# Kernel tuning notes

Measured on AMD Instinct MI355X. Metric: run time of the kernel, lower is better.

Reference implementation:

```python
import jax, jax.numpy as jnp
import numpy as np
import math

D_MODEL = 512; NHEAD = 8; D_HEAD = 64; C_OUT = 64
SEQ_LEN = 1024; PRED_LEN = 256; K = 8; DIM_FF = 2048
LOW_FREQ = 1; EPS = 1e-5
BATCH = 8


def _next_fast_len(n):
    # smallest 5-smooth integer >= n (matches scipy.fftpack.next_fast_len)
    while True:
        m = n
        for p in (2, 3, 5):
            while m % p == 0:
                m //= p
        if m == 1:
            return n
        n += 1


def _conv1d_fft(f, g, n):
    # matches torch conv1d_fft with N == M == n along axis 1 (cross-correlation via conj)
    fast_len = _next_fast_len(2 * n - 1)
    Ff = jnp.fft.rfft(f, n=fast_len, axis=1)
    Fg = jnp.fft.rfft(g, n=fast_len, axis=1)
    out = jnp.fft.irfft(Ff * jnp.conj(Fg), n=fast_len, axis=1)
    out = jnp.roll(out, -1, axis=1)
    return out[:, fast_len - n:fast_len]


def _exp_smooth(values, sw, v0, aux_values=None):
    # values: (b,t,h,d); sw: (h,1); v0: (1,1,h,d or 1)
    b, t, h, d = values.shape
    alpha = jax.nn.sigmoid(sw)                        # (h,1)
    powers = jnp.arange(t, dtype=values.dtype)
    weight = (1.0 - alpha) * alpha ** powers[::-1]    # (h,t)
    init_w = alpha ** (powers + 1.0)                  # (h,t)
    weight = weight.T[None, :, :, None]               # (1,t,h,1)
    init_w = init_w.T[None, :, :, None]
    out = init_w * v0 + _conv1d_fft(values, weight, t)
    if aux_values is not None:
        aux_w = weight * (alpha / (1.0 - alpha))[None, None, :, :]
        out = out + _conv1d_fft(aux_values, aux_w, t)
    return out


def _layer_norm(x, g, b):
    mu = x.mean(-1, keepdims=True)
    var = ((x - mu) ** 2).mean(-1, keepdims=True)
    return (x - mu) * jax.lax.rsqrt(var + EPS) * g + b


def _fourier_season(x):
    b, t, d = x.shape
    xf = jnp.fft.rfft(x, axis=1)                      # (b, t//2+1, d) complex
    hi = xf.shape[1] - 1 if t % 2 == 0 else xf.shape[1]
    xf = xf[:, LOW_FREQ:hi]                           # (b, F, d)
    freqs = (jnp.arange(t // 2 + 1, dtype=x.dtype) / t)[LOW_FREQ:hi]
    # top-K frequencies per (batch, feature) by amplitude
    _, idx = jax.lax.top_k(jnp.abs(jnp.moveaxis(xf, 1, 2)), K)   # (b,d,K)
    idx = jnp.moveaxis(idx, 2, 1)                     # (b,K,d)
    x_sel = jnp.take_along_axis(xf, idx, axis=1)      # (b,K,d) complex
    f_sel = freqs[idx]                                # (b,K,d)
    # trig re-synthesis / extrapolation over t + PRED_LEN steps
    x_all = jnp.concatenate([x_sel, jnp.conj(x_sel)], axis=1)    # (b,2K,d)
    f_all = jnp.concatenate([f_sel, -f_sel], axis=1)[:, :, None, :]  # (b,2K,1,d)
    t_val = jnp.arange(t + PRED_LEN, dtype=x.dtype).reshape(1, 1, -1, 1)
    amp = (jnp.abs(x_all) / t)[:, :, None, :]
    phase = jnp.angle(x_all)[:, :, None, :]
    x_time = amp * jnp.cos(2.0 * math.pi * f_all * t_val + phase)  # (b,2K,T,d)
    return x_time.sum(axis=1)                         # (b, t+PRED_LEN, d)


def _growth_layer(x, z0, in_w, in_b, sw, v0, out_w, out_b):
    b, t, _ = x.shape
    v = (x @ in_w.T + in_b).reshape(b, t, NHEAD, D_HEAD)
    v = jnp.concatenate([jnp.broadcast_to(z0[None, None], (b, 1, NHEAD, D_HEAD)), v], axis=1)
    v = v[:, 1:] - v[:, :-1]                          # first differences, (b,t,h,dh)
    s = _exp_smooth(v, sw, v0)
    s = jnp.concatenate([jnp.broadcast_to(v0, (b, 1, NHEAD, D_HEAD)), s], axis=1)  # (b,t+1,h,dh)
    return s.reshape(b, t + 1, NHEAD * D_HEAD) @ out_w.T + out_b


def _level_layer(level, growth, season, sw, v0, gw, gb, spw, spb):
    b, t, _ = level.shape
    g = (growth @ gw.T + gb)[..., None]               # (b,t,c,1)
    s = (season @ spw.T + spb)[..., None]             # (b,t,c,1)
    l = level[..., None] - s
    out = _exp_smooth(l, sw, v0, aux_values=g)        # (b,t,c,1)
    return out[..., 0]


def _forward(res, level, gl_z0, gl_in_w, gl_in_b, gl_sw, gl_v0, gl_out_w, gl_out_b,
             ll_sw, ll_v0, ll_gw, ll_gb, ll_sw2, ll_sb, ff_w1, ff_w2,
             n1_g, n1_b, n2_g, n2_b):
    season = _fourier_season(res)                     # (b, t+P, d)
    res = res - season[:, :-PRED_LEN]
    growth = _growth_layer(res, gl_z0, gl_in_w, gl_in_b, gl_sw, gl_v0, gl_out_w, gl_out_b)  # (b,t+1,d)
    res = _layer_norm(res - growth[:, 1:], n1_g, n1_b)
    ff = jax.nn.sigmoid(res @ ff_w1.T) @ ff_w2.T      # Feedforward, activation='sigmoid', no bias
    res = _layer_norm(res + ff, n2_g, n2_b)
    level = _level_layer(level, growth[:, :-1], season[:, :-PRED_LEN],
                         ll_sw, ll_v0, ll_gw, ll_gb, ll_sw2, ll_sb)
    return res, level, growth, season


def setup_inputs() -> dict:
    key = jax.random.key(0)
    ks = jax.random.split(key, 16)
    f32 = jnp.float32
    rn = lambda k, shape, s=1.0: jax.random.normal(k, shape, dtype=f32) * s
    return {
        "res": rn(ks[0], (BATCH, SEQ_LEN, D_MODEL)),
        "level": rn(ks[1], (BATCH, SEQ_LEN, C_OUT)),
        "gl_z0": rn(ks[2], (NHEAD, D_HEAD)),
        "gl_in_w": rn(ks[3], (NHEAD * D_HEAD, D_MODEL), 0.02),
        "gl_in_b": jnp.zeros((NHEAD * D_HEAD,), f32),
        "gl_sw": rn(ks[4], (NHEAD, 1)),
        "gl_v0": rn(ks[5], (1, 1, NHEAD, D_HEAD)),
        "gl_out_w": rn(ks[6], (D_MODEL, NHEAD * D_HEAD), 0.02),
        "gl_out_b": jnp.zeros((D_MODEL,), f32),
        "ll_sw": rn(ks[7], (C_OUT, 1)),
        "ll_v0": rn(ks[8], (1, 1, C_OUT, 1)),
        "ll_gw": rn(ks[9], (C_OUT, D_MODEL), 0.02),
        "ll_gb": jnp.zeros((C_OUT,), f32),
        "ll_sw2": rn(ks[10], (C_OUT, D_MODEL), 0.02),
        "ll_sb": jnp.zeros((C_OUT,), f32),
        "ff_w1": rn(ks[11], (DIM_FF, D_MODEL), 0.02),
        "ff_w2": rn(ks[12], (D_MODEL, DIM_FF), 0.02),
        "n1_g": jnp.ones((D_MODEL,), f32),
        "n1_b": jnp.zeros((D_MODEL,), f32),
        "n2_g": jnp.ones((D_MODEL,), f32),
        "n2_b": jnp.zeros((D_MODEL,), f32),
    }


def reference(res, level, gl_z0, gl_in_w, gl_in_b, gl_sw, gl_v0, gl_out_w, gl_out_b,
              ll_sw, ll_v0, ll_gw, ll_gb, ll_sw2, ll_sb, ff_w1, ff_w2,
              n1_g, n1_b, n2_g, n2_b):
    return _forward(res, level, gl_z0, gl_in_w, gl_in_b, gl_sw, gl_v0, gl_out_w, gl_out_b,
                    ll_sw, ll_v0, ll_gw, ll_gb, ll_sw2, ll_sb, ff_w1, ff_w2,
                    n1_g, n1_b, n2_g, n2_b)
```

## Files before the change

### kernel.cpp

```cpp
#include <hip/hip_runtime.h>
#include <hip/hip_bf16.h>
#include <math.h>

#define B_ 8
#define T_ 1024
#define D_ 512
#define PRED 256
#define TP (T_ + PRED)
#define NH 8
#define DH 64
#define DFF 2048
#define CO 64
#define KSEL 8

typedef __hip_bfloat16 bf16;
using bf16x8 = __attribute__((ext_vector_type(8))) short;
using f32x4  = __attribute__((ext_vector_type(4))) float;

__device__ __forceinline__ void gload_lds16(const void* gp, void* lp) {
  __builtin_amdgcn_global_load_lds(
      (const __attribute__((address_space(1))) void*)gp,
      (__attribute__((address_space(3))) void*)lp, 16, 0, 0);
}

template <int N>
__device__ __forceinline__ void vm_wait() {
  if constexpr (N == 0)      asm volatile("s_waitcnt vmcnt(0)" ::: "memory");
  else if constexpr (N == 2) asm volatile("s_waitcnt vmcnt(2)" ::: "memory");
  else if constexpr (N == 4) asm volatile("s_waitcnt vmcnt(4)" ::: "memory");
  else if constexpr (N == 6) asm volatile("s_waitcnt vmcnt(6)" ::: "memory");
  else if constexpr (N == 8) asm volatile("s_waitcnt vmcnt(8)" ::: "memory");
  else static_assert(N == 0, "unsupported vmcnt literal");
}

__global__ __launch_bounds__(256) void k_transpose(const float* __restrict__ in, float* __restrict__ out) {
  __shared__ float tile[32][33];
  const int b = blockIdx.z;
  const int d0 = blockIdx.x * 32, t0 = blockIdx.y * 32;
  const int tx = threadIdx.x, ty = threadIdx.y;
  const float* src = in + ((size_t)b * T_ + t0) * D_ + d0;
#pragma unroll
  for (int i = 0; i < 32; i += 8) tile[ty + i][tx] = src[(size_t)(ty + i) * D_ + tx];
  __syncthreads();
  float* dst = out + ((size_t)b * D_ + d0) * T_ + t0;
#pragma unroll
  for (int i = 0; i < 32; i += 8) dst[(size_t)(ty + i) * T_ + tx] = tile[tx][ty + i];
}

__global__ __launch_bounds__(256) void k_fft_topk(const float* __restrict__ xt, float* __restrict__ comp) {
  __shared__ float2 bufA[2][512], bufB[2][512];
  __shared__ float2 tw[384];
  __shared__ float wvv[2][2][4];
  __shared__ int wkk[2][2][4];
  __shared__ int selk[2][KSEL];
  float* const mg0 = (float*)&bufA[0][0];
  float* const mg1 = (float*)&bufA[1][0];
  const int j = threadIdx.x;
  const size_t bd0 = (size_t)blockIdx.x * 2;
  {
    const float c = -6.283185307179586f / 512.0f;
    tw[j] = make_float2(__cosf(c * (float)j), __sinf(c * (float)j));
    if (j < 128) tw[256 + j] = make_float2(__cosf(c * (float)(256 + j)), __sinf(c * (float)(256 + j)));
  }
  const float4 u0 = ((const float4*)(xt + bd0 * 1024))[j];
  const float4 u1 = ((const float4*)(xt + (bd0 + 1) * 1024))[j];
  bufA[0][2 * j] = make_float2(u0.x, u0.y); bufA[0][2 * j + 1] = make_float2(u0.z, u0.w);
  bufA[1][2 * j] = make_float2(u1.x, u1.y); bufA[1][2 * j + 1] = make_float2(u1.z, u1.w);
  __syncthreads();
  {
    const float2 w = tw[j];
#pragma unroll
    for (int sx2 = 0; sx2 < 2; ++sx2) {
      const float2 a = bufA[sx2][j], b = bufA[sx2][j + 256];
      bufB[sx2][2 * j] = make_float2(a.x + b.x, a.y + b.y);
      const float ex = a.x - b.x, ey = a.y - b.y;
      bufB[sx2][2 * j + 1] = make_float2(ex * w.x - ey * w.y, ex * w.y + ey * w.x);
    }
  }
  __syncthreads();
  const int sx = j >> 7, idx = j & 127;
#pragma unroll
  for (int st = 0; st < 4; ++st) {
    const int lg = 1 + 2 * st;
    const int s = 1 << lg;
    const int p = idx >> lg;
    const int q = idx & (s - 1);
    const float2* src = (st & 1) ? (const float2*)bufA[sx] : (const float2*)bufB[sx];
    float2* dst = (st & 1) ? (float2*)bufB[sx] : (float2*)bufA[sx];
    const float2 x0 = src[idx];
    const float2 x1 = src[idx + 128];
    const float2 x2 = src[idx + 256];
    const float2 x3 = src[idx + 384];
    const float2 e0 = make_float2(x0.x + x2.x, x0.y + x2.y);
    const float2 e1 = make_float2(x0.x - x2.x, x0.y - x2.y);
    const float2 e2 = make_float2(x1.x + x3.x, x1.y + x3.y);
    const float2 e3 = make_float2(x1.x - x3.x, x1.y - x3.y);
    const float2 y0 = make_float2(e0.x + e2.x, e0.y + e2.y);
    const float2 y2 = make_float2(e0.x - e2.x, e0.y - e2.y);
    const float2 y1 = make_float2(e1.x + e3.y, e1.y - e3.x);
    const float2 y3 = make_float2(e1.x - e3.y, e1.y + e3.x);
    const int spi = p << lg;
    const float2 w1 = tw[spi], w2 = tw[2 * spi], w3 = tw[3 * spi];
    const int ob = q + (p << (lg + 2));
    dst[ob] = y0;
    dst[ob + s] = make_float2(y1.x * w1.x - y1.y * w1.y, y1.x * w1.y + y1.y * w1.x);
    dst[ob + 2 * s] = make_float2(y2.x * w2.x - y2.y * w2.y, y2.x * w2.y + y2.y * w2.x);
    dst[ob + 3 * s] = make_float2(y3.x * w3.x - y3.y * w3.y, y3.x * w3.y + y3.y * w3.x);
    __syncthreads();
  }
#pragma unroll
  for (int u = 0; u < 2; ++u) {
    const int k = (u == 0) ? (j + 1) : (j + 257);
    if (k <= 511) {
#pragma unroll
      for (int s2 = 0; s2 < 2; ++s2) {
        const float2 zk = bufB[s2][k & 511];
        const float2 zm = bufB[s2][(512 - k) & 511];
        const float Ex = 0.5f * (zk.x + zm.x), Ey = 0.5f * (zk.y - zm.y);
        const float Ox = 0.5f * (zk.y + zm.y), Oy = 0.5f * (zm.x - zk.x);
        const float ang = -(6.283185307179586f / 1024.0f) * (float)k;
        const float cs = __cosf(ang), sn = __sinf(ang);
        const float Xr = Ex + cs * Ox - sn * Oy;
        const float Xi = Ey + cs * Oy + sn * Ox;
        ((s2 == 0) ? mg0 : mg1)[k] = Xr * Xr + Xi * Xi;
      }
    }
  }
  __syncthreads();
  float a0 = mg0[j], b0v = mg0[j + 256];
  float a1 = mg1[j], b1v = mg1[j + 256];
  if (j == 0) { a0 = -1.0f; a1 = -1.0f; }
  const int lane = j & 63, wvi = j >> 6;
  for (int r = 0; r < KSEL; ++r) {
    const int par = r & 1;
    float bv0 = a0; int bk0 = j;
    if (b0v > bv0) { bv0 = b0v; bk0 = j + 256; }
    float bv1 = a1; int bk1 = j;
    if (b1v > bv1) { bv1 = b1v; bk1 = j + 256; }
#pragma unroll
    for (int off = 32; off; off >>= 1) {
      const float ov0 = __shfl_down(bv0, off); const int ok0 = __shfl_down(bk0, off);
      if (ov0 > bv0 || (ov0 == bv0 && ok0 < bk0)) { bv0 = ov0; bk0 = ok0; }
      const float ov1 = __shfl_down(bv1, off); const int ok1 = __shfl_down(bk1, off);
      if (ov1 > bv1 || (ov1 == bv1 && ok1 < bk1)) { bv1 = ov1; bk1 = ok1; }
    }
    if (lane == 0) {
      wvv[0][par][wvi] = bv0; wkk[0][par][wvi] = bk0;
      wvv[1][par][wvi] = bv1; wkk[1][par][wvi] = bk1;
    }
    __syncthreads();
    float fv0 = wvv[0][par][0]; int fk0 = wkk[0][par][0];
    float fv1 = wvv[1][par][0]; int fk1 = wkk[1][par][0];
#pragma unroll
    for (int i = 1; i < 4; i++) {
      if (wvv[0][par][i] > fv0 || (wvv[0][par][i] == fv0 && wkk[0][par][i] < fk0)) { fv0 = wvv[0][par][i]; fk0 = wkk[0][par][i]; }
      if (wvv[1][par][i] > fv1 || (wvv[1][par][i] == fv1 && wkk[1][par][i] < fk1)) { fv1 = wvv[1][par][i]; fk1 = wkk[1][par][i]; }
    }
    if (j == 0) { selk[0][r] = fk0; selk[1][r] = fk1; }
    if (fk0 == j) a0 = -2.0f;
    if (fk0 == j + 256) b0v = -2.0f;
    if (fk1 == j) a1 = -2.0f;
    if (fk1 == j + 256) b1v = -2.0f;
  }
  __syncthreads();
  if (j < 2 * KSEL) {
    const int s2 = j >> 3, r = j & 7;
    const int k = selk[s2][r];
    const float2 zk = bufB[s2][k & 511];
    const float2 zm = bufB[s2][(512 - k) & 511];
    const float Ex = 0.5f * (zk.x + zm.x), Ey = 0.5f * (zk.y - zm.y);
    const float Ox = 0.5f * (zk.y + zm.y), Oy = 0.5f * (zm.x - zk.x);
    const float ang = -(6.283185307179586f / 1024.0f) * (float)k;
    const float cs = __cosf(ang), sn = __sinf(ang);
    const float Xr = Ex + cs * Ox - sn * Oy;
    const float Xi = Ey + cs * Oy + sn * Ox;
    float* o = comp + (bd0 + s2) * 24 + r * 3;
    o[0] = 2.0f * sqrtf(Xr * Xr + Xi * Xi) * (1.0f / 1024.0f);
    o[1] = (float)k;
    o[2] = atan2f(Xi, Xr);
  }
}

__global__ __launch_bounds__(512) void k_season(const float* __restrict__ comp, const float* __restrict__ res,
                                                float* __restrict__ season, bf16* __restrict__ res1b,
                                                bf16* __restrict__ seasb) {
  const int d = threadIdx.x;
  const int b = blockIdx.y;
  const int t0 = blockIdx.x * 5;
  float a_[8], kf_[8], ph_[8];
  const float* c = comp + ((size_t)b * 512 + d) * 24;
#pragma unroll
  for (int i = 0; i < 8; i++) { a_[i] = c[3 * i]; kf_[i] = c[3 * i + 1]; ph_[i] = c[3 * i + 2]; }
#pragma unroll
  for (int tt = 0; tt < 5; ++tt) {
    const int t = t0 + tt;
    float acc = 0.0f;
#pragma unroll
    for (int i = 0; i < 8; i++) {
      float fr = kf_[i] * (float)t * (1.0f / 1024.0f);
      fr -= floorf(fr);
      acc += a_[i] * __cosf(fmaf(6.283185307179586f, fr, ph_[i]));
    }
    season[((size_t)b * TP + t) * D_ + d] = acc;
    if (t < T_) {
      const float rr = res[((size_t)b * T_ + t) * D_ + d] - acc;
      res1b[((size_t)b * T_ + t) * D_ + d] = __float2bfloat16(rr);
      seasb[((size_t)b * T_ + t) * D_ + d] = __float2bfloat16(acc);
    }
  }
}

#define CVT_TOTAL 2686976
__global__ __launch_bounds__(256) void k_cvt_all(const float* __restrict__ s0, const float* __restrict__ s1,
                                                 const float* __restrict__ s2_, const float* __restrict__ s3,
                                                 const float* __restrict__ s4, const float* __restrict__ s5,
                                                 bf16* __restrict__ dst) {
  const int i = (blockIdx.x * 256 + threadIdx.x) * 4;
  if (i >= CVT_TOTAL) return;
  const float* src;
  int off;
  if (i < 262144)       { src = s0;  off = i; }
  else if (i < 524288)  { src = s1;  off = i - 262144; }
  else if (i < 1572864) { src = s2_; off = i - 524288; }
  else if (i < 2621440) { src = s3;  off = i - 1572864; }
  else if (i < 2654208) { src = s4;  off = i - 2621440; }
  else                  { src = s5;  off = i - 2654208; }
  const float4 v = *(const float4*)(src + off);
  bf16* o = dst + i;
  o[0] = __float2bfloat16(v.x); o[1] = __float2bfloat16(v.y);
  o[2] = __float2bfloat16(v.z); o[3] = __float2bfloat16(v.w);
}

__global__ __launch_bounds__(1024) void k_growth_scan2(const float* __restrict__ v, const float* __restrict__ z0,
                                                       const float* __restrict__ sw, const float* __restrict__ v0,
                                                       bf16* __restrict__ s2) {
  const int b = blockIdx.x >> 3;
  const int col = (blockIdx.x & 7) * 64 + (threadIdx.x & 63);
  const int w = threadIdx.x >> 6;
  const float alpha = 1.0f / (1.0f + expf(-sw[col >> 6]));
  const float om = 1.0f - alpha;
  float a64 = alpha;
#pragma unroll
  for (int i = 0; i < 6; i++) a64 *= a64;
  const float* vp = v + (size_t)b * T_ * D_ + col;
  float vprev = (w == 0) ? z0[col] : vp[(size_t)(64 * w - 1) * D_];
  float sloc = 0.0f;
#pragma unroll 8
  for (int j = 0; j < 64; j++) {
    const float nv = vp[(size_t)(64 * w + j) * D_];
    sloc = alpha * sloc + om * (nv - vprev);
    vprev = nv;
  }
  __shared__ float lb[16][64], lc[16][64];
  lb[w][threadIdx.x & 63] = sloc;
  __syncthreads();
  if (w == 0) {
    float s = v0[col];
#pragma unroll
    for (int k = 0; k < 16; k++) { lc[k][threadIdx.x & 63] = s; s = a64 * s + lb[k][threadIdx.x & 63]; }
  }
  __syncthreads();
  float s = lc[w][threadIdx.x & 63];
  vprev = (w == 0) ? z0[col] : vp[(size_t)(64 * w - 1) * D_];
  bf16* op = s2 + (size_t)b * (T_ + 1) * D_ + col;
  if (w == 0) op[0] = __float2bfloat16(v0[col]);
#pragma unroll 8
  for (int j = 0; j < 64; j++) {
    const float nv = vp[(size_t)(64 * w + j) * D_];
    s = alpha * s + om * (nv - vprev);
    vprev = nv;
    op[(size_t)(64 * w + j + 1) * D_] = __float2bfloat16(s);
  }
}

__global__ __launch_bounds__(1024) void k_level_scan2(const float* __restrict__ level, const float* __restrict__ gp,
                                                      const float* __restrict__ sp, const float* __restrict__ sw,
                                                      const float* __restrict__ v0, float* __restrict__ out) {
  const int b = blockIdx.x;
  const int w = threadIdx.x >> 6;
  const int c = threadIdx.x & 63;
  const float alpha = 1.0f / (1.0f + expf(-sw[c]));
  const float om = 1.0f - alpha;
  float a64 = alpha;
#pragma unroll
  for (int i = 0; i < 6; i++) a64 *= a64;
  const size_t base = ((size_t)b * T_ + 64 * w) * CO + c;
  float sloc = 0.0f;
#pragma unroll 8
  for (int j = 0; j < 64; j++) {
    const size_t idx = base + (size_t)j * CO;
    const float u = om * (level[idx] - sp[idx]) + alpha * gp[idx];
    out[idx] = u;
    sloc = alpha * sloc + u;
  }
  __shared__ float lb[16][64], lc[16][64];
  lb[w][c] = sloc;
  __syncthreads();
  if (w == 0) {
    float s = v0[c];
#pragma unroll
    for (int k = 0; k < 16; k++) { lc[k][c] = s; s = a64 * s + lb[k][c]; }
  }
  __syncthreads();
  float s = lc[w][c];
#pragma unroll 8
  for (int j = 0; j < 64; j++) {
    const size_t idx = base + (size_t)j * CO;
    s = alpha * s + out[idx];
    out[idx] = s;
  }
}

template <int MODE>
__global__ __launch_bounds__(128) void k_ln(const float* __restrict__ x1, const bf16* __restrict__ xb,
                                            const float* __restrict__ x3, const float* __restrict__ g,
                                            const float* __restrict__ be, float* __restrict__ outF,
                                            bf16* __restrict__ outB) {
  const int m = blockIdx.x, tid = threadIdx.x;
  const int b = m >> 10;
  float4 v;
  if (MODE == 0) {
    const ushort4 rb = ((const ushort4*)(xb + (size_t)m * D_))[tid];
    const float4 gr = ((const float4*)(x3 + ((size_t)(m + b + 1)) * D_))[tid];
    v.x = __uint_as_float((unsigned)rb.x << 16) - gr.x;
    v.y = __uint_as_float((unsigned)rb.y << 16) - gr.y;
    v.z = __uint_as_float((unsigned)rb.z << 16) - gr.z;
    v.w = __uint_as_float((unsigned)rb.w << 16) - gr.w;
  } else {
    v = ((const float4*)(x1 + (size_t)m * D_))[tid];
  }
  float s = v.x + v.y + v.z + v.w;
  float s2 = v.x * v.x + v.y * v.y + v.z * v.z + v.w * v.w;
#pragma unroll
  for (int off = 32; off; off >>= 1) { s += __shfl_down(s, off); s2 += __shfl_down(s2, off); }
  __shared__ float p1[2], p2[2];
  if ((tid & 63) == 0) { p1[tid >> 6] = s; p2[tid >> 6] = s2; }
  __syncthreads();
  const float S = p1[0] + p1[1], S2 = p2[0] + p2[1];
  const float mu = S * (1.0f / 512.0f);
  const float rs = rsqrtf(fmaxf(S2 * (1.0f / 512.0f) - mu * mu, 0.0f) + 1e-5f);
  const float4 gg = ((const float4*)g)[tid], bb = ((const float4*)be)[tid];
  float4 o;
  o.x = (v.x - mu) * rs * gg.x + bb.x;
  o.y = (v.y - mu) * rs * gg.y + bb.y;
  o.z = (v.z - mu) * rs * gg.z + bb.z;
  o.w = (v.w - mu) * rs * gg.w + bb.w;
  ((float4*)(outF + (size_t)m * D_))[tid] = o;
  if (MODE == 0) {
    bf16* ob = outB + (size_t)m * D_ + tid * 4;
    ob[0] = __float2bfloat16(o.x); ob[1] = __float2bfloat16(o.y);
    ob[2] = __float2bfloat16(o.z); ob[3] = __float2bfloat16(o.w);
  }
}

template <int BM, int BN, int BK, int WM, int WN, int EPI, bool DUAL = false>
__global__ __launch_bounds__(WM * WN * 64, 2) void k_gemm(
    const bf16* __restrict__ A, const bf16* __restrict__ Bw,
    const float* __restrict__ bias, float* outF, bf16* __restrict__ outB,
    const float* resid, const int M, const int N, const int K, int extra,
    const bf16* __restrict__ A2, const bf16* __restrict__ Bw2,
    const float* __restrict__ bias2, float* outF2, int extra2) {
  constexpr int NW = WM * WN;
  constexpr int FM = BM / (WM * 16);
  constexpr int FN = BN / (WN * 16);
  constexpr int RPC = 512 / BK;
  constexpr int LA = (BM / RPC) / NW, LB = (BN / RPC) / NW;
  constexpr int KK = BK / 32;
  constexpr int TLOADS = LA + LB;
  static_assert(LA >= 1 && LB >= 1, "tile too small for staging split");
  static_assert((BM / RPC) % NW == 0 && (BN / RPC) % NW == 0, "staging split");
  if constexpr (DUAL) {
    if (blockIdx.z == 1) { A = A2; Bw = Bw2; bias = bias2; outF = outF2; extra = extra2; }
  }
  __shared__ bf16 lsA[2][BM * BK];
  __shared__ bf16 lsB[2][BN * BK];
  const int tid = threadIdx.x;
  const int w = tid >> 6, lane = tid & 63;
  const int tm = blockIdx.x, tn = blockIdx.y;
  const int wr = w / WN, wc = w % WN;
  const int r16 = lane & 15, hi = lane >> 4;

  int srowoff, scoloff;
  if constexpr (BK == 64) {
    const int rr = lane >> 3, cs = lane & 7;
    srowoff = rr;
    scoloff = (cs ^ rr) * 8;
  } else {
    const int sr = lane >> 3, cs = lane & 7;
    const int idx = cs ^ (sr & 7);
    srowoff = sr * 2 + (idx >> 2);
    scoloff = (idx & 3) * 8;
  }

  const f32x4 fzero = {0.f, 0.f, 0.f, 0.f};
  f32x4 acc[FM][FN];
#pragma unroll
  for (int i = 0; i < FM; i++)
#pragma unroll
    for (int jj = 0; jj < FN; jj++) acc[i][jj] = fzero;

  const int NT = K / BK;

  auto stage = [&](int kt, int sel) {
#pragma unroll
    for (int q = 0; q < LA; q++) {
      const int g = w * LA + q;
      int m = tm * BM + g * RPC + srowoff;
      if (m > M - 1) m = M - 1;
      m += (m >> 10) * extra;
      gload_lds16(A + (size_t)m * K + (size_t)kt * BK + scoloff, &lsA[sel][g * 512]);
    }
#pragma unroll
    for (int q = 0; q < LB; q++) {
      const int g = w * LB + q;
      const int n = tn * BN + g * RPC + srowoff;
      gload_lds16(Bw + (size_t)n * K + (size_t)kt * BK + scoloff, &lsB[sel][g * 512]);
    }
  };

  auto frag = [&](const bf16* ls, int row, int cc) -> bf16x8 {
    if constexpr (BK == 64) {
      const int g = row >> 3, rr = row & 7;
      return *(const bf16x8*)&ls[g * 512 + rr * 64 + ((cc ^ rr) << 3)];
    } else {
      const int g = row >> 4, rr = row & 15, sr = rr >> 1;
      const int idx = ((rr & 1) << 2) | cc;
      return *(const bf16x8*)&ls[g * 512 + sr * 64 + ((idx ^ (sr & 7)) << 3)];
    }
  };

  stage(0, 0);
  for (int kt = 0; kt < NT; ++kt) {
    const int sel = kt & 1;
    if (kt + 1 < NT) {
      stage(kt + 1, sel ^ 1);
      vm_wait<TLOADS>();
    } else {
      vm_wait<0>();
    }
    __builtin_amdgcn_sched_barrier(0);
    __builtin_amdgcn_s_barrier();
    __builtin_amdgcn_sched_barrier(0);
#pragma unroll
    for (int kk = 0; kk < KK; ++kk) {
      bf16x8 af[FM], bfv[FN];
#pragma unroll
      for (int i = 0; i < FM; i++)
        af[i] = frag(lsA[sel], wr * (FM * 16) + i * 16 + r16, kk * 4 + hi);
#pragma unroll
      for (int jj = 0; jj < FN; jj++)
        bfv[jj] = frag(lsB[sel], wc * (FN * 16) + jj * 16 + r16, kk * 4 + hi);
#pragma unroll
      for (int i = 0; i < FM; i++)
#pragma unroll
        for (int jj = 0; jj < FN; jj++)
          acc[i][jj] = __builtin_amdgcn_mfma_f32_16x16x32_bf16(af[i], bfv[jj], acc[i][jj], 0, 0, 0);
    }
    if (kt + 1 < NT) {
      __builtin_amdgcn_sched_barrier(0);
      __builtin_amdgcn_s_barrier();
      __builtin_amdgcn_sched_barrier(0);
    }
  }

#pragma unroll
  for (int i = 0; i < FM; i++) {
#pragma unroll
    for (int r = 0; r < 4; r++) {
      const int m = tm * BM + wr * (FM * 16) + i * 16 + hi * 4 + r;
      if (m < M) {
#pragma unroll
        for (int jj = 0; jj < FN; jj++) {
          const int n = tn * BN + wc * (FN * 16) + jj * 16 + r16;
          float x = acc[i][jj][r];
          if (bias) x += bias[n];
          const size_t idx = (size_t)m * N + n;
          if (EPI == 0) {
            outF[idx] = x;
          } else if (EPI == 1) {
            outF[idx] = x;
            outB[idx] = __float2bfloat16(x);
          } else if (EPI == 2) {
            outB[idx] = __float2bfloat16(1.0f / (1.0f + __expf(-x)));
          } else {
            outF[idx] = x + resid[idx];
          }
        }
      }
    }
  }
}

#define MB (size_t)(1u << 20)
static const size_t OFF_A = 0;
static const size_t OFF_C = 32 * MB;
static const size_t OFF_D = 40 * MB;
static const size_t OFF_E = 48 * MB;
static const size_t OFF_F = 54 * MB;
static const size_t OFF_G = 63 * MB;
static const size_t OFF_H = 72 * MB;
static const size_t OFF_J = 88 * MB;
static const size_t OFF_K = 89 * MB;
static const size_t OFF_K2 = 91 * MB;

#define W_IN 0
#define W_OUT 262144
#define W_FF1 524288
#define W_FF2 1572864
#define W_GW 2621440
#define W_SW2 2654208

extern "C" void kernel_launch(void* const* d_in, const int* in_sizes, int n_in, void* d_out, int out_size,
                              void* d_ws, size_t ws_size, hipStream_t stream) {
  (void)in_sizes; (void)n_in; (void)out_size; (void)ws_size;
  const float* res = (const float*)d_in[0];
  const float* level = (const float*)d_in[1];
  const float* gl_z0 = (const float*)d_in[2];
  const float* gl_in_w = (const float*)d_in[3];
  const float* gl_in_b = (const float*)d_in[4];
  const float* gl_sw = (const float*)d_in[5];
  const float* gl_v0 = (const float*)d_in[6];
  const float* gl_out_w = (const float*)d_in[7];
  const float* gl_out_b = (const float*)d_in[8];
  const float* ll_sw = (const float*)d_in[9];
  const float* ll_v0 = (const float*)d_in[10];
  const float* ll_gw = (const float*)d_in[11];
  const float* ll_gb = (const float*)d_in[12];
  const float* ll_sw2 = (const float*)d_in[13];
  const float* ll_sb = (const float*)d_in[14];
  const float* ff_w1 = (const float*)d_in[15];
  const float* ff_w2 = (const float*)d_in[16];
  const float* n1_g = (const float*)d_in[17];
  const float* n1_b = (const float*)d_in[18];
  const float* n2_g = (const float*)d_in[19];
  const float* n2_b = (const float*)d_in[20];

  char* ws = (char*)d_ws;
  float* resT = (float*)(ws + OFF_A);
  float* vbuf = (float*)(ws + OFF_A);
  bf16* hbuf = (bf16*)(ws + OFF_A);
  bf16* res1b = (bf16*)(ws + OFF_C);
  bf16* res2b = (bf16*)(ws + OFF_C);
  bf16* seasb = (bf16*)(ws + OFF_D);
  bf16* wE = (bf16*)(ws + OFF_E);
  bf16* s2b = (bf16*)(ws + OFF_F);
  bf16* grob = (bf16*)(ws + OFF_G);
  float* res2f = (float*)(ws + OFF_H);
  float* comp = (float*)(ws + OFF_J);
  float* gproj = (float*)(ws + OFF_K);
  float* sproj = (float*)(ws + OFF_K2);

  float* o_res = (float*)d_out;
  float* o_level = o_res + 4194304;
  float* o_growth = o_level + 524288;
  float* o_season = o_growth + 4198400;

  k_transpose<<<dim3(16, 32, 8), dim3(32, 8), 0, stream>>>(res, resT);
  k_fft_topk<<<2048, 256, 0, stream>>>(resT, comp);
  k_season<<<dim3(256, 8), 512, 0, stream>>>(comp, res, o_season, res1b, seasb);
  k_cvt_all<<<(CVT_TOTAL / 4 + 255) / 256, 256, 0, stream>>>(gl_in_w, gl_out_w, ff_w1, ff_w2, ll_gw, ll_sw2, wE);
  k_gemm<64, 128, 64, 2, 2, 0><<<dim3(128, 4), 256, 0, stream>>>(
      res1b, wE + W_IN, gl_in_b, vbuf, nullptr, nullptr, 8192, 512, 512, 0,
      nullptr, nullptr, nullptr, nullptr, 0);
  k_growth_scan2<<<64, 1024, 0, stream>>>(vbuf, gl_z0, gl_sw, gl_v0, s2b);
  k_gemm<64, 128, 64, 2, 2, 1><<<dim3(129, 4), 256, 0, stream>>>(
      s2b, wE + W_OUT, gl_out_b, o_growth, grob, nullptr, 8200, 512, 512, 0,
      nullptr, nullptr, nullptr, nullptr, 0);
  k_ln<0><<<8192, 128, 0, stream>>>(nullptr, res1b, o_growth, n1_g, n1_b, res2f, res2b);
  k_gemm<128, 128, 32, 2, 2, 2><<<dim3(64, 16), 256, 0, stream>>>(
      res2b, wE + W_FF1, nullptr, nullptr, hbuf, nullptr, 8192, 2048, 512, 0,
      nullptr, nullptr, nullptr, nullptr, 0);
  k_gemm<64, 128, 64, 2, 2, 3><<<dim3(128, 4), 256, 0, stream>>>(
      hbuf, wE + W_FF2, nullptr, res2f, nullptr, res2f, 8192, 512, 2048, 0,
      nullptr, nullptr, nullptr, nullptr, 0);
  k_ln<1><<<8192, 128, 0, stream>>>(res2f, nullptr, nullptr, n2_g, n2_b, o_res, nullptr);
  k_gemm<64, 64, 64, 4, 1, 0, true><<<dim3(128, 1, 2), 256, 0, stream>>>(
      grob, wE + W_GW, ll_gb, gproj, nullptr, nullptr, 8192, 64, 512, 1,
      seasb, wE + W_SW2, ll_sb, sproj, 0);
  k_level_scan2<<<8, 1024, 0, stream>>>(level, gproj, sproj, ll_sw, ll_v0, o_level);
}
```

Baseline: 216.4 us.

## Fuse level-layer dual projections into one concatenated-K GEMM with folded scaling

The growth and season bf16 activations are written interleaved into one buffer of row width 1024, and the two projection weights are concatenated along K, pre-scaled by alpha and -(1-alpha). A single K=1024 GEMM with a new epilogue then computes the level-smoothing input u directly. This removes the second GEMM half, the separate gproj/sproj buffers and the first-pass elementwise work in the level scan. LayerNorm 1 now reads the growth output as bf16 from the shared buffer rather than fp32, which cuts read traffic but adds rounding.

```diff
diff --git a/kernel.cpp b/kernel.cpp
--- a/kernel.cpp
+++ b/kernel.cpp
@@ -183,7 +183,7 @@
 
 __global__ __launch_bounds__(512) void k_season(const float* __restrict__ comp, const float* __restrict__ res,
                                                 float* __restrict__ season, bf16* __restrict__ res1b,
-                                                bf16* __restrict__ seasb) {
+                                                bf16* __restrict__ seasC) {
   const int d = threadIdx.x;
   const int b = blockIdx.y;
   const int t0 = blockIdx.x * 5;
@@ -205,7 +205,7 @@
     if (t < T_) {
       const float rr = res[((size_t)b * T_ + t) * D_ + d] - acc;
       res1b[((size_t)b * T_ + t) * D_ + d] = __float2bfloat16(rr);
-      seasb[((size_t)b * T_ + t) * D_ + d] = __float2bfloat16(acc);
+      seasC[((size_t)b * 1025 + t) * 1024 + 512 + d] = __float2bfloat16(acc);
     }
   }
 }
@@ -214,21 +214,33 @@
 __global__ __launch_bounds__(256) void k_cvt_all(const float* __restrict__ s0, const float* __restrict__ s1,
                                                  const float* __restrict__ s2_, const float* __restrict__ s3,
                                                  const float* __restrict__ s4, const float* __restrict__ s5,
-                                                 bf16* __restrict__ dst) {
+                                                 const float* __restrict__ llsw, bf16* __restrict__ dst) {
   const int i = (blockIdx.x * 256 + threadIdx.x) * 4;
   if (i >= CVT_TOTAL) return;
   const float* src;
   int off;
+  float scale = 1.0f;
+  int di = i;
   if (i < 262144)       { src = s0;  off = i; }
   else if (i < 524288)  { src = s1;  off = i - 262144; }
   else if (i < 1572864) { src = s2_; off = i - 524288; }
   else if (i < 2621440) { src = s3;  off = i - 1572864; }
-  else if (i < 2654208) { src = s4;  off = i - 2621440; }
-  else                  { src = s5;  off = i - 2654208; }
+  else if (i < 2654208) {
+    src = s4;  off = i - 2621440;
+    const int c = off >> 9, k = off & 511;
+    scale = 1.0f / (1.0f + __expf(-llsw[c]));
+    di = 2621440 + c * 1024 + k;
+  } else {
+    src = s5;  off = i - 2654208;
+    const int c = off >> 9, k = off & 511;
+    const float alpha = 1.0f / (1.0f + __expf(-llsw[c]));
+    scale = -(1.0f - alpha);
+    di = 2621440 + c * 1024 + 512 + k;
+  }
   const float4 v = *(const float4*)(src + off);
-  bf16* o = dst + i;
-  o[0] = __float2bfloat16(v.x); o[1] = __float2bfloat16(v.y);
-  o[2] = __float2bfloat16(v.z); o[3] = __float2bfloat16(v.w);
+  bf16* o = dst + di;
+  o[0] = __float2bfloat16(v.x * scale); o[1] = __float2bfloat16(v.y * scale);
+  o[2] = __float2bfloat16(v.z * scale); o[3] = __float2bfloat16(v.w * scale);
 }
 
 __global__ __launch_bounds__(1024) void k_growth_scan2(const float* __restrict__ v, const float* __restrict__ z0,
@@ -273,26 +285,19 @@
   }
 }
 
-__global__ __launch_bounds__(1024) void k_level_scan2(const float* __restrict__ level, const float* __restrict__ gp,
-                                                      const float* __restrict__ sp, const float* __restrict__ sw,
+__global__ __launch_bounds__(1024) void k_level_scan2(const float* __restrict__ ubuf, const float* __restrict__ sw,
                                                       const float* __restrict__ v0, float* __restrict__ out) {
   const int b = blockIdx.x;
   const int w = threadIdx.x >> 6;
   const int c = threadIdx.x & 63;
   const float alpha = 1.0f / (1.0f + expf(-sw[c]));
-  const float om = 1.0f - alpha;
   float a64 = alpha;
 #pragma unroll
   for (int i = 0; i < 6; i++) a64 *= a64;
   const size_t base = ((size_t)b * T_ + 64 * w) * CO + c;
   float sloc = 0.0f;
 #pragma unroll 8
-  for (int j = 0; j < 64; j++) {
-    const size_t idx = base + (size_t)j * CO;
-    const float u = om * (level[idx] - sp[idx]) + alpha * gp[idx];
-    out[idx] = u;
-    sloc = alpha * sloc + u;
-  }
+  for (int j = 0; j < 64; j++) sloc = alpha * sloc + ubuf[base + (size_t)j * CO];
   __shared__ float lb[16][64], lc[16][64];
   lb[w][c] = sloc;
   __syncthreads();
@@ -306,14 +311,14 @@
 #pragma unroll 8
   for (int j = 0; j < 64; j++) {
     const size_t idx = base + (size_t)j * CO;
-    s = alpha * s + out[idx];
+    s = alpha * s + ubuf[idx];
     out[idx] = s;
   }
 }
 
 template <int MODE>
 __global__ __launch_bounds__(128) void k_ln(const float* __restrict__ x1, const bf16* __restrict__ xb,
-                                            const float* __restrict__ x3, const float* __restrict__ g,
+                                            const bf16* __restrict__ x3, const float* __restrict__ g,
                                             const float* __restrict__ be, float* __restrict__ outF,
                                             bf16* __restrict__ outB) {
   const int m = blockIdx.x, tid = threadIdx.x;
@@ -321,11 +326,11 @@
   float4 v;
   if (MODE == 0) {
     const ushort4 rb = ((const ushort4*)(xb + (size_t)m * D_))[tid];
-    const float4 gr = ((const float4*)(x3 + ((size_t)(m + b + 1)) * D_))[tid];
-    v.x = __uint_as_float((unsigned)rb.x << 16) - gr.x;
-    v.y = __uint_as_float((unsigned)rb.y << 16) - gr.y;
-    v.z = __uint_as_float((unsigned)rb.z << 16) - gr.z;
-    v.w = __uint_as_float((unsigned)rb.w << 16) - gr.w;
+    const ushort4 gr = ((const ushort4*)(x3 + ((size_t)(m + b + 1)) * 1024))[tid];
+    v.x = __uint_as_float((unsigned)rb.x << 16) - __uint_as_float((unsigned)gr.x << 16);
+    v.y = __uint_as_float((unsigned)rb.y << 16) - __uint_as_float((unsigned)gr.y << 16);
+    v.z = __uint_as_float((unsigned)rb.z << 16) - __uint_as_float((unsigned)gr.z << 16);
+    v.w = __uint_as_float((unsigned)rb.w << 16) - __uint_as_float((unsigned)gr.w << 16);
   } else {
     v = ((const float4*)(x1 + (size_t)m * D_))[tid];
   }
@@ -353,13 +358,12 @@
   }
 }
 
-template <int BM, int BN, int BK, int WM, int WN, int EPI, bool DUAL = false>
+template <int BM, int BN, int BK, int WM, int WN, int EPI>
 __global__ __launch_bounds__(WM * WN * 64, 2) void k_gemm(
     const bf16* __restrict__ A, const bf16* __restrict__ Bw,
     const float* __restrict__ bias, float* outF, bf16* __restrict__ outB,
-    const float* resid, const int M, const int N, const int K, int extra,
-    const bf16* __restrict__ A2, const bf16* __restrict__ Bw2,
-    const float* __restrict__ bias2, float* outF2, int extra2) {
+    const float* resid, const int M, const int N, const int K, const int extra, const int obst,
+    const float* __restrict__ sw4, const float* __restrict__ gb4, const float* __restrict__ sb4) {
   constexpr int NW = WM * WN;
   constexpr int FM = BM / (WM * 16);
   constexpr int FN = BN / (WN * 16);
@@ -369,9 +373,6 @@
   constexpr int TLOADS = LA + LB;
   static_assert(LA >= 1 && LB >= 1, "tile too small for staging split");
   static_assert((BM / RPC) % NW == 0 && (BN / RPC) % NW == 0, "staging split");
-  if constexpr (DUAL) {
-    if (blockIdx.z == 1) { A = A2; Bw = Bw2; bias = bias2; outF = outF2; extra = extra2; }
-  }
   __shared__ bf16 lsA[2][BM * BK];
   __shared__ bf16 lsB[2][BN * BK];
   const int tid = threadIdx.x;
@@ -479,11 +480,15 @@
             outF[idx] = x;
           } else if (EPI == 1) {
             outF[idx] = x;
-            outB[idx] = __float2bfloat16(x);
+            outB[(size_t)m * obst + n] = __float2bfloat16(x);
           } else if (EPI == 2) {
-            outB[idx] = __float2bfloat16(1.0f / (1.0f + __expf(-x)));
+            outB[(size_t)m * obst + n] = __float2bfloat16(1.0f / (1.0f + __expf(-x)));
+          } else if (EPI == 3) {
+            outF[idx] = x + resid[idx];
           } else {
-            outF[idx] = x + resid[idx];
+            const float a = 1.0f / (1.0f + __expf(-sw4[n]));
+            const float om = 1.0f - a;
+            outF[idx] = x + a * gb4[n] - om * sb4[n] + om * resid[idx];
           }
         }
       }
@@ -494,21 +499,18 @@
 #define MB (size_t)(1u << 20)
 static const size_t OFF_A = 0;
 static const size_t OFF_C = 32 * MB;
-static const size_t OFF_D = 40 * MB;
-static const size_t OFF_E = 48 * MB;
-static const size_t OFF_F = 54 * MB;
-static const size_t OFF_G = 63 * MB;
+static const size_t OFF_E = 40 * MB;
+static const size_t OFF_F = 46 * MB;
+static const size_t OFF_G = 55 * MB;
 static const size_t OFF_H = 72 * MB;
 static const size_t OFF_J = 88 * MB;
 static const size_t OFF_K = 89 * MB;
-static const size_t OFF_K2 = 91 * MB;
 
 #define W_IN 0
 #define W_OUT 262144
 #define W_FF1 524288
 #define W_FF2 1572864
 #define W_GW 2621440
-#define W_SW2 2654208
 
 extern "C" void kernel_launch(void* const* d_in, const int* in_sizes, int n_in, void* d_out, int out_size,
                               void* d_ws, size_t ws_size, hipStream_t stream) {
@@ -541,14 +543,12 @@
   bf16* hbuf = (bf16*)(ws + OFF_A);
   bf16* res1b = (bf16*)(ws + OFF_C);
   bf16* res2b = (bf16*)(ws + OFF_C);
-  bf16* seasb = (bf16*)(ws + OFF_D);
   bf16* wE = (bf16*)(ws + OFF_E);
   bf16* s2b = (bf16*)(ws + OFF_F);
-  bf16* grob = (bf16*)(ws + OFF_G);
+  bf16* agC = (bf16*)(ws + OFF_G);
   float* res2f = (float*)(ws + OFF_H);
   float* comp = (float*)(ws + OFF_J);
-  float* gproj = (float*)(ws + OFF_K);
-  float* sproj = (float*)(ws + OFF_K2);
+  float* ubuf = (float*)(ws + OFF_K);
 
   float* o_res = (float*)d_out;
   float* o_level = o_res + 4194304;
@@ -557,25 +557,25 @@
 
   k_transpose<<<dim3(16, 32, 8), dim3(32, 8), 0, stream>>>(res, resT);
   k_fft_topk<<<2048, 256, 0, stream>>>(resT, comp);
-  k_season<<<dim3(256, 8), 512, 0, stream>>>(comp, res, o_season, res1b, seasb);
-  k_cvt_all<<<(CVT_TOTAL / 4 + 255) / 256, 256, 0, stream>>>(gl_in_w, gl_out_w, ff_w1, ff_w2, ll_gw, ll_sw2, wE);
+  k_season<<<dim3(256, 8), 512, 0, stream>>>(comp, res, o_season, res1b, agC);
+  k_cvt_all<<<(CVT_TOTAL / 4 + 255) / 256, 256, 0, stream>>>(gl_in_w, gl_out_w, ff_w1, ff_w2, ll_gw, ll_sw2, ll_sw, wE);
   k_gemm<64, 128, 64, 2, 2, 0><<<dim3(128, 4), 256, 0, stream>>>(
-      res1b, wE + W_IN, gl_in_b, vbuf, nullptr, nullptr, 8192, 512, 512, 0,
-      nullptr, nullptr, nullptr, nullptr, 0);
+      res1b, wE + W_IN, gl_in_b, vbuf, nullptr, nullptr, 8192, 512, 512, 0, 512,
+      nullptr, nullptr, nullptr);
   k_growth_scan2<<<64, 1024, 0, stream>>>(vbuf, gl_z0, gl_sw, gl_v0, s2b);
   k_gemm<64, 128, 64, 2, 2, 1><<<dim3(129, 4), 256, 0, stream>>>(
-      s2b, wE + W_OUT, gl_out_b, o_growth, grob, nullptr, 8200, 512, 512, 0,
-      nullptr, nullptr, nullptr, nullptr, 0);
-  k_ln<0><<<8192, 128, 0, stream>>>(nullptr, res1b, o_growth, n1_g, n1_b, res2f, res2b);
+      s2b, wE + W_OUT, gl_out_b, o_growth, agC, nullptr, 8200, 512, 512, 0, 1024,
+      nullptr, nullptr, nullptr);
+  k_ln<0><<<8192, 128, 0, stream>>>(nullptr, res1b, agC, n1_g, n1_b, res2f, res2b);
   k_gemm<128, 128, 32, 2, 2, 2><<<dim3(64, 16), 256, 0, stream>>>(
-      res2b, wE + W_FF1, nullptr, nullptr, hbuf, nullptr, 8192, 2048, 512, 0,
-      nullptr, nullptr, nullptr, nullptr, 0);
+      res2b, wE + W_FF1, nullptr, nullptr, hbuf, nullptr, 8192, 2048, 512, 0, 2048,
+      nullptr, nullptr, nullptr);
   k_gemm<64, 128, 64, 2, 2, 3><<<dim3(128, 4), 256, 0, stream>>>(
-      hbuf, wE + W_FF2, nullptr, res2f, nullptr, res2f, 8192, 512, 2048, 0,
-      nullptr, nullptr, nullptr, nullptr, 0);
+      hbuf, wE + W_FF2, nullptr, res2f, nullptr, res2f, 8192, 512, 2048, 0, 512,
+      nullptr, nullptr, nullptr);
   k_ln<1><<<8192, 128, 0, stream>>>(res2f, nullptr, nullptr, n2_g, n2_b, o_res, nullptr);
-  k_gemm<64, 64, 64, 4, 1, 0, true><<<dim3(128, 1, 2), 256, 0, stream>>>(
-      grob, wE + W_GW, ll_gb, gproj, nullptr, nullptr, 8192, 64, 512, 1,
-      seasb, wE + W_SW2, ll_sb, sproj, 0);
-  k_level_scan2<<<8, 1024, 0, stream>>>(level, gproj, sproj, ll_sw, ll_v0, o_level);
-}
+  k_gemm<64, 64, 64, 4, 1, 4><<<dim3(128, 1), 256, 0, stream>>>(
+      agC, wE + W_GW, nullptr, ubuf, nullptr, level, 8192, 64, 1024, 1, 64,
+      ll_sw, ll_gb, ll_sb);
+  k_level_scan2<<<8, 1024, 0, stream>>>(ubuf, ll_sw, ll_v0, o_level);
+}
```

Result: no change. 215.2 us (-0.6%).
